# Kernel optimization log

Measured on AMD Instinct MI355X. Metric: run time of the kernel, lower is better.

## Reference

```python
import jax, jax.numpy as jnp
import numpy as np

GRID = 256
N_PTS = 500000

# 8 trilinear corner offsets
_OFFSETS = jnp.array([[0,0,0],[1,0,0],[0,1,0],[1,1,0],
                      [0,0,1],[1,0,1],[0,1,1],[1,1,1]], dtype=jnp.int32)


def setup_inputs() -> dict:
    key = jax.random.key(0)
    k1, k2 = jax.random.split(key)
    # match model init: means ~ N(0, 0.1), weights = |N(0,1)| (rand>=0 is equivalent post-relu)
    means = jax.random.normal(k1, (N_PTS, 3), dtype=jnp.float32) * 0.1
    weights = jax.random.uniform(k2, (N_PTS,), dtype=jnp.float32)
    sigma_param = jnp.ones((1,), dtype=jnp.float32)
    return {"means": means, "weights": weights, "sigma_param": sigma_param}


def _splat_trilinear(means, weights, grid_shape):
    factor = 0.5 * grid_shape
    grid_coords = means * factor + factor                      # [N,3]
    base = jax.lax.stop_gradient(jnp.floor(grid_coords).astype(jnp.int32))
    rem = grid_coords - base                                   # [N,3]
    # corner weights: prod over xyz of (rem if offset==1 else 1-rem) -> [N,8]
    terms = jnp.where(_OFFSETS[None, :, :] == 1, rem[:, None, :], 1.0 - rem[:, None, :])
    corner_w = jnp.prod(terms, axis=-1)                        # [N,8]
    vals = (corner_w * weights[:, None]).reshape(-1)           # [8N]
    idx = (base[:, None, :] + _OFFSETS[None, :, :]).reshape(-1, 3)  # [8N,3]
    grid = jnp.zeros((grid_shape, grid_shape, grid_shape), dtype=jnp.float32)
    # out-of-bounds indices are dropped by jax default scatter mode (same as original)
    return grid.at[idx[:, 0], idx[:, 1], idx[:, 2]].add(vals)


def _fft_blur(vol, sigma, grid_shape):
    d = h = w = grid_shape
    fz = jnp.fft.fftfreq(d)[:, None, None]
    fy = jnp.fft.fftfreq(h)[None, :, None]
    fx = jnp.fft.rfftfreq(w)[None, None, :]
    f_sq = (fz**2 + fy**2 + fx**2).astype(jnp.float32)         # [D,H,W//2+1]
    mask = jnp.exp(-2.0 * jnp.pi**2 * sigma**2 * f_sq)
    x = vol[None, ..., None]                                   # NDHWC
    spectrum = jnp.fft.rfftn(x, axes=(1, 2, 3))
    filtered = spectrum * mask[None, ..., None]
    out = jnp.fft.irfftn(filtered, s=(d, h, w), axes=(1, 2, 3))
    return out[0, ..., 0]


def reference(means, weights, sigma_param):
    w = jax.nn.relu(weights)
    sigma = jax.nn.relu(sigma_param)
    vol = _splat_trilinear(means, w, GRID)
    return _fft_blur(vol, sigma, GRID)
```

## Files before the change

kernel.cpp:

```cpp
#include <hip/hip_runtime.h>
#include <math.h>

#define GN 256
#define VOLN (GN * GN * GN)
#define VOLBYTES ((size_t)VOLN * sizeof(float))
#define RAD 16

#define CELLW 16
#define CPA   16
#define CELLS (CPA * CPA * CPA)
#define TILEW (CELLW + 1)
#define TILEN (TILEW * TILEW * TILEW)

#define HB  512
#define PPT 2
#define CHUNK 2048
#define MAXCHUNKS 4352

#define CCH 16

__device__ __forceinline__ int cell_of(float g0, float g1, float g2) {
    int b0 = (int)floorf(g0), b1 = (int)floorf(g1), b2 = (int)floorf(g2);
    b0 = min(max(b0, 0), 255); b1 = min(max(b1, 0), 255); b2 = min(max(b2, 0), 255);
    return ((b0 >> 4) << 8) | ((b1 >> 4) << 4) | (b2 >> 4);
}

__global__ __launch_bounds__(HB) void hist_kernel(const float* __restrict__ means,
                                                  unsigned* __restrict__ cellcnt, int n) {
    __shared__ unsigned lh[CELLS];
    int t = threadIdx.x;
    for (int i = t; i < CELLS; i += HB) lh[i] = 0u;
    __syncthreads();
    int base = blockIdx.x * (HB * PPT);
    for (int j = 0; j < PPT; ++j) {
        int p = base + j * HB + t;
        if (p < n) {
            float g0 = fmaf(means[3 * p + 0], 128.f, 128.f);
            float g1 = fmaf(means[3 * p + 1], 128.f, 128.f);
            float g2 = fmaf(means[3 * p + 2], 128.f, 128.f);
            atomicAdd(&lh[cell_of(g0, g1, g2)], 1u);
        }
    }
    __syncthreads();
    for (int i = t; i < CELLS; i += HB) {
        unsigned v = lh[i];
        if (v) atomicAdd(&cellcnt[i], v);
    }
}

__global__ __launch_bounds__(1024) void scan_kernel(const unsigned* __restrict__ cellcnt,
                                                    unsigned* __restrict__ cellstart,
                                                    unsigned* __restrict__ cursor,
                                                    uint4* __restrict__ desc) {
    __shared__ unsigned sums[1024];
    int t = threadIdx.x;
    unsigned c[4], loc[4], tot = 0u;
#pragma unroll
    for (int i = 0; i < 4; ++i) { c[i] = cellcnt[t * 4 + i]; loc[i] = tot; tot += c[i]; }
    sums[t] = tot;
    __syncthreads();
    for (int ofs = 1; ofs < 1024; ofs <<= 1) {
        unsigned v = (t >= ofs) ? sums[t - ofs] : 0u;
        __syncthreads();
        sums[t] += v;
        __syncthreads();
    }
    unsigned base = (t == 0) ? 0u : sums[t - 1];
    unsigned cs[4];
#pragma unroll
    for (int i = 0; i < 4; ++i) {
        cs[i] = base + loc[i];
        cellstart[t * 4 + i] = cs[i];
        cursor[t * 4 + i] = cs[i];
    }
    unsigned nch[4], lch[4], ctot = 0u;
#pragma unroll
    for (int i = 0; i < 4; ++i) { nch[i] = (c[i] + CHUNK - 1) / CHUNK; lch[i] = ctot; ctot += nch[i]; }
    __syncthreads();
    sums[t] = ctot;
    __syncthreads();
    for (int ofs = 1; ofs < 1024; ofs <<= 1) {
        unsigned v = (t >= ofs) ? sums[t - ofs] : 0u;
        __syncthreads();
        sums[t] += v;
        __syncthreads();
    }
    unsigned cbase = (t == 0) ? 0u : sums[t - 1];
#pragma unroll
    for (int i = 0; i < 4; ++i) {
        unsigned cb = cbase + lch[i];
        for (unsigned k = 0; k < nch[i]; ++k) {
            unsigned s0 = cs[i] + k * CHUNK;
            unsigned s1 = min(s0 + CHUNK, cs[i] + c[i]);
            desc[cb + k] = make_uint4((unsigned)(t * 4 + i), s0, s1, 0u);
        }
    }
    __syncthreads();
    unsigned total = sums[1023];
    for (unsigned i = total + t; i < MAXCHUNKS; i += 1024)
        desc[i] = make_uint4(0xFFFFFFFFu, 0u, 0u, 0u);
}

__global__ __launch_bounds__(HB) void scatter_kernel(const float* __restrict__ means,
                                                     const float* __restrict__ weights,
                                                     unsigned* __restrict__ cursor,
                                                     float4* __restrict__ sorted, int n) {
    __shared__ unsigned lh[CELLS];
    int t = threadIdx.x;
    for (int i = t; i < CELLS; i += HB) lh[i] = 0u;
    __syncthreads();
    int base = blockIdx.x * (HB * PPT);
    for (int j = 0; j < PPT; ++j) {
        int p = base + j * HB + t;
        if (p < n) {
            float g0 = fmaf(means[3 * p + 0], 128.f, 128.f);
            float g1 = fmaf(means[3 * p + 1], 128.f, 128.f);
            float g2 = fmaf(means[3 * p + 2], 128.f, 128.f);
            atomicAdd(&lh[cell_of(g0, g1, g2)], 1u);
        }
    }
    __syncthreads();
    for (int i = t; i < CELLS; i += HB) {
        unsigned v = lh[i];
        lh[i] = v ? atomicAdd(&cursor[i], v) : 0u;
    }
    __syncthreads();
    for (int j = 0; j < PPT; ++j) {
        int p = base + j * HB + t;
        if (p < n) {
            float g0 = fmaf(means[3 * p + 0], 128.f, 128.f);
            float g1 = fmaf(means[3 * p + 1], 128.f, 128.f);
            float g2 = fmaf(means[3 * p + 2], 128.f, 128.f);
            unsigned pos = atomicAdd(&lh[cell_of(g0, g1, g2)], 1u);
            sorted[pos] = make_float4(g0, g1, g2, fmaxf(weights[p], 0.f));
        }
    }
}

__global__ __launch_bounds__(256) void cellsplat_kernel(const float4* __restrict__ sorted,
                                                        const uint4* __restrict__ desc,
                                                        float* __restrict__ vol) {
    __shared__ float tile[TILEN];
    uint4 d = desc[blockIdx.x];
    if (d.x == 0xFFFFFFFFu) return;
    int c = (int)d.x;
    unsigned start = d.y, end = d.z;
    for (int i = threadIdx.x; i < TILEN; i += 256) tile[i] = 0.f;
    __syncthreads();
    int cb0 = (c >> 8) << 4, cb1 = ((c >> 4) & 15) << 4, cb2 = (c & 15) << 4;
    for (unsigned p0 = start; p0 < end; p0 += 256) {
        unsigned p = p0 + threadIdx.x;
        if (p < end) {
            float4 q = sorted[p];
            float f0 = floorf(q.x), f1 = floorf(q.y), f2 = floorf(q.z);
            int b0 = (int)f0, b1 = (int)f1, b2 = (int)f2;
            float r0 = q.x - f0, r1 = q.y - f1, r2 = q.z - f2;
            float c0v[2] = {1.f - r0, r0}, c1v[2] = {1.f - r1, r1}, c2v[2] = {1.f - r2, r2};
#pragma unroll
            for (int o0 = 0; o0 < 2; ++o0) {
                int v0 = b0 + o0, t0 = v0 - cb0;
                if ((unsigned)t0 > 16u || (unsigned)v0 > 255u) continue;
#pragma unroll
                for (int o1 = 0; o1 < 2; ++o1) {
                    int v1 = b1 + o1, t1 = v1 - cb1;
                    if ((unsigned)t1 > 16u || (unsigned)v1 > 255u) continue;
                    float w01 = c0v[o0] * c1v[o1] * q.w;
#pragma unroll
                    for (int o2 = 0; o2 < 2; ++o2) {
                        int v2 = b2 + o2, t2 = v2 - cb2;
                        if ((unsigned)t2 > 16u || (unsigned)v2 > 255u) continue;
                        atomicAdd(&tile[t0 * (TILEW * TILEW) + t1 * TILEW + t2], w01 * c2v[o2]);
                    }
                }
            }
        }
    }
    __syncthreads();
    for (int i = threadIdx.x; i < TILEN; i += 256) {
        float val = tile[i];
        if (val == 0.f) continue;
        int t0 = i / (TILEW * TILEW);
        int rem = i - t0 * (TILEW * TILEW);
        int t1 = rem / TILEW, t2 = rem - t1 * TILEW;
        int v0 = cb0 + t0, v1 = cb1 + t1, v2 = cb2 + t2;
        if (v0 < 256 && v1 < 256 && v2 < 256)
            atomicAdd(&vol[(v0 << 16) | (v1 << 8) | v2], val);
    }
}

__global__ __launch_bounds__(256) void taps_kernel(const float* __restrict__ sigma_param,
                                                   float* __restrict__ h) {
    __shared__ float red[4];
    int k = threadIdx.x;
    float s = fmaxf(sigma_param[0], 0.f);
    int kk = (k < 128) ? k : k - 256;
    float f = (float)kk / 256.f;
    float cc = 2.f * (float)(M_PI * M_PI) * s * s;
    float term = expf(-cc * f * f);
    int wid = k >> 6, lane = k & 63;
    for (int m = 0; m <= RAD; ++m) {
        int idx = (k * m) & 255;
        float v = term * cosf((float)idx * (2.f * (float)M_PI / 256.f));
#pragma unroll
        for (int o = 32; o > 0; o >>= 1) v += __shfl_down(v, o, 64);
        if (lane == 0) red[wid] = v;
        __syncthreads();
        if (k == 0) h[m] = (red[0] + red[1] + red[2] + red[3]) * (1.f / 256.f);
        __syncthreads();
    }
}

__global__ __launch_bounds__(256) void conv_d0_kernel(const float* __restrict__ in,
                                                      float* __restrict__ out,
                                                      const float* __restrict__ hh) {
    __shared__ float4 tile4[96][CCH];
    float shv[17];
#pragma unroll
    for (int j = 0; j < 17; ++j) shv[j] = hh[j];
    float taps[33];
#pragma unroll
    for (int m = 0; m < 33; ++m) taps[m] = shv[m < 16 ? 16 - m : m - 16];
    int i1 = blockIdx.x, t0 = blockIdx.y, ch = blockIdx.z;
    int colbase4 = ch * CCH;
    const float4* in4 = (const float4*)in;
#pragma unroll
    for (int it = 0; it < (96 * CCH) / 256; ++it) {
        int e = it * 256 + threadIdx.x;
        int r = e / CCH, cc = e % CCH;
        int i0 = ((t0 << 6) + r - 16) & 255;
        tile4[r][cc] = in4[(i0 << 14) | (i1 << 6) | (colbase4 + cc)];
    }
    __syncthreads();
    int cg = threadIdx.x & (CCH - 1);
    int r0 = threadIdx.x / CCH;
    for (int ro = 0; ro < 4; ++ro) {
        int rr = r0 + ro * 16;
        float4 acc = make_float4(0.f, 0.f, 0.f, 0.f);
#pragma unroll
        for (int m = 0; m < 33; ++m) {
            float4 v = tile4[rr + m][cg];
            acc.x = fmaf(taps[m], v.x, acc.x);
            acc.y = fmaf(taps[m], v.y, acc.y);
            acc.z = fmaf(taps[m], v.z, acc.z);
            acc.w = fmaf(taps[m], v.w, acc.w);
        }
        int o0 = (t0 << 6) + rr;
        ((float4*)out)[(o0 << 14) | (i1 << 6) | (colbase4 + cg)] = acc;
    }
}

__global__ __launch_bounds__(256) void conv_d1_kernel(const float* __restrict__ in,
                                                      float* __restrict__ out,
                                                      const float* __restrict__ hh) {
    __shared__ float4 tile4[96][CCH];
    float shv[17];
#pragma unroll
    for (int j = 0; j < 17; ++j) shv[j] = hh[j];
    float taps[33];
#pragma unroll
    for (int m = 0; m < 33; ++m) taps[m] = shv[m < 16 ? 16 - m : m - 16];
    int i0 = blockIdx.x, t1 = blockIdx.y, ch = blockIdx.z;
    int colbase4 = ch * CCH;
    const float4* in4 = (const float4*)in;
#pragma unroll
    for (int it = 0; it < (96 * CCH) / 256; ++it) {
        int e = it * 256 + threadIdx.x;
        int r = e / CCH, cc = e % CCH;
        int i1 = ((t1 << 6) + r - 16) & 255;
        tile4[r][cc] = in4[(i0 << 14) | (i1 << 6) | (colbase4 + cc)];
    }
    __syncthreads();
    int cg = threadIdx.x & (CCH - 1);
    int r0 = threadIdx.x / CCH;
    for (int ro = 0; ro < 4; ++ro) {
        int rr = r0 + ro * 16;
        float4 acc = make_float4(0.f, 0.f, 0.f, 0.f);
#pragma unroll
        for (int m = 0; m < 33; ++m) {
            float4 v = tile4[rr + m][cg];
            acc.x = fmaf(taps[m], v.x, acc.x);
            acc.y = fmaf(taps[m], v.y, acc.y);
            acc.z = fmaf(taps[m], v.z, acc.z);
            acc.w = fmaf(taps[m], v.w, acc.w);
        }
        int o1 = (t1 << 6) + rr;
        ((float4*)out)[(i0 << 14) | (o1 << 6) | (colbase4 + cg)] = acc;
    }
}

__global__ __launch_bounds__(256) void conv_d2_kernel(const float* __restrict__ in,
                                                      float* __restrict__ out,
                                                      const float* __restrict__ hh) {
    __shared__ float tile[4][256];
    float shv[17];
#pragma unroll
    for (int j = 0; j < 17; ++j) shv[j] = hh[j];
    int bx = blockIdx.x;
    size_t base = (size_t)bx * 1024;
#pragma unroll
    for (int it = 0; it < 4; ++it) {
        int e = it * 256 + threadIdx.x;
        ((float*)tile)[e] = in[base + e];
    }
    __syncthreads();
    int ri = threadIdx.x >> 6;
    int k = threadIdx.x & 63;
    const float4* row4 = (const float4*)tile[ri];
    float w[36];
#pragma unroll
    for (int j = 0; j < 9; ++j) {
        float4 q = row4[(k - 4 + j) & 63];
        w[4 * j + 0] = q.x; w[4 * j + 1] = q.y; w[4 * j + 2] = q.z; w[4 * j + 3] = q.w;
    }
    float acc[4] = {0.f, 0.f, 0.f, 0.f};
#pragma unroll
    for (int kk = 0; kk < 36; ++kk) {
#pragma unroll
        for (int i = 0; i < 4; ++i) {
            int d = kk - 16 - i;
            if (d >= -16 && d <= 16) acc[i] = fmaf(shv[d < 0 ? -d : d], w[kk], acc[i]);
        }
    }
    ((float4*)out)[(size_t)bx * 256 + ri * 64 + k] = make_float4(acc[0], acc[1], acc[2], acc[3]);
}

extern "C" void kernel_launch(void* const* d_in, const int* in_sizes, int n_in,
                              void* d_out, int out_size, void* d_ws, size_t ws_size,
                              hipStream_t stream) {
    const float* means   = (const float*)d_in[0];
    const float* weights = (const float*)d_in[1];
    const float* sigma   = (const float*)d_in[2];
    int n = in_sizes[1];

    float* vol = (float*)d_ws;
    float* h   = (float*)((char*)d_ws + VOLBYTES);
    float* out = (float*)d_out;

    char* ob = (char*)d_out;
    float4*   sorted    = (float4*)ob;
    unsigned* cellcnt   = (unsigned*)(ob + (8u << 20));
    unsigned* cellstart = (unsigned*)(ob + (8u << 20) + 65536);
    unsigned* cursor    = (unsigned*)(ob + (8u << 20) + 131072);
    uint4*    desc      = (uint4*)(ob + (9u << 20));

    hipMemsetAsync(vol, 0, VOLBYTES, stream);
    hipMemsetAsync(cellcnt, 0, CELLS * sizeof(unsigned), stream);
    taps_kernel<<<1, 256, 0, stream>>>(sigma, h);

    int nb = (n + HB * PPT - 1) / (HB * PPT);
    hist_kernel<<<nb, HB, 0, stream>>>(means, cellcnt, n);
    scan_kernel<<<1, 1024, 0, stream>>>(cellcnt, cellstart, cursor, desc);
    scatter_kernel<<<nb, HB, 0, stream>>>(means, weights, cursor, sorted, n);
    cellsplat_kernel<<<MAXCHUNKS, 256, 0, stream>>>(sorted, desc, vol);

    conv_d0_kernel<<<dim3(256, 4, 4), 256, 0, stream>>>(vol, out, h);
    conv_d1_kernel<<<dim3(256, 4, 4), 256, 0, stream>>>(out, vol, h);
    conv_d2_kernel<<<16384, 256, 0, stream>>>(vol, out, h);
}
```

Before: 244.9 us.

## Register-block depth convolutions over 8 outputs and widen cellsplat blocks

The d0/d1 convolution kernels now have each thread compute 8 consecutive outputs in registers, sliding over 40 shared-memory rows. This replaces 33 shared loads per output with 5 per output, which reduces LDS traffic. The tile is widened to 32 float4 columns and the grid z-dimension is halved to match. Cellsplat now launches 1024-thread blocks so each block processes more points at once. The cost is higher register pressure from 8 float4 accumulators plus 33 taps, and larger blocks in cellsplat may lower occupancy or increase contention on shared-memory atomics.

```diff
diff --git a/kernel.cpp b/kernel.cpp
--- a/kernel.cpp
+++ b/kernel.cpp
@@ -16,8 +16,9 @@
 #define PPT 2
 #define CHUNK 2048
 #define MAXCHUNKS 4352
-
-#define CCH 16
+#define SB  1024
+
+#define CCH 32
 
 __device__ __forceinline__ int cell_of(float g0, float g1, float g2) {
     int b0 = (int)floorf(g0), b1 = (int)floorf(g1), b2 = (int)floorf(g2);
@@ -137,18 +138,18 @@
     }
 }
 
-__global__ __launch_bounds__(256) void cellsplat_kernel(const float4* __restrict__ sorted,
-                                                        const uint4* __restrict__ desc,
-                                                        float* __restrict__ vol) {
+__global__ __launch_bounds__(SB) void cellsplat_kernel(const float4* __restrict__ sorted,
+                                                       const uint4* __restrict__ desc,
+                                                       float* __restrict__ vol) {
     __shared__ float tile[TILEN];
     uint4 d = desc[blockIdx.x];
     if (d.x == 0xFFFFFFFFu) return;
     int c = (int)d.x;
     unsigned start = d.y, end = d.z;
-    for (int i = threadIdx.x; i < TILEN; i += 256) tile[i] = 0.f;
+    for (int i = threadIdx.x; i < TILEN; i += SB) tile[i] = 0.f;
     __syncthreads();
     int cb0 = (c >> 8) << 4, cb1 = ((c >> 4) & 15) << 4, cb2 = (c & 15) << 4;
-    for (unsigned p0 = start; p0 < end; p0 += 256) {
+    for (unsigned p0 = start; p0 < end; p0 += SB) {
         unsigned p = p0 + threadIdx.x;
         if (p < end) {
             float4 q = sorted[p];
@@ -176,7 +177,7 @@
         }
     }
     __syncthreads();
-    for (int i = threadIdx.x; i < TILEN; i += 256) {
+    for (int i = threadIdx.x; i < TILEN; i += SB) {
         float val = tile[i];
         if (val == 0.f) continue;
         int t0 = i / (TILEW * TILEW);
@@ -226,26 +227,34 @@
 #pragma unroll
     for (int it = 0; it < (96 * CCH) / 256; ++it) {
         int e = it * 256 + threadIdx.x;
-        int r = e / CCH, cc = e % CCH;
+        int r = e >> 5, cc = e & 31;
         int i0 = ((t0 << 6) + r - 16) & 255;
         tile4[r][cc] = in4[(i0 << 14) | (i1 << 6) | (colbase4 + cc)];
     }
     __syncthreads();
-    int cg = threadIdx.x & (CCH - 1);
-    int r0 = threadIdx.x / CCH;
-    for (int ro = 0; ro < 4; ++ro) {
-        int rr = r0 + ro * 16;
-        float4 acc = make_float4(0.f, 0.f, 0.f, 0.f);
-#pragma unroll
-        for (int m = 0; m < 33; ++m) {
-            float4 v = tile4[rr + m][cg];
-            acc.x = fmaf(taps[m], v.x, acc.x);
-            acc.y = fmaf(taps[m], v.y, acc.y);
-            acc.z = fmaf(taps[m], v.z, acc.z);
-            acc.w = fmaf(taps[m], v.w, acc.w);
-        }
-        int o0 = (t0 << 6) + rr;
-        ((float4*)out)[(o0 << 14) | (i1 << 6) | (colbase4 + cg)] = acc;
+    int cg = threadIdx.x & 31;
+    int b = (threadIdx.x >> 5) << 3;
+    float4 acc[8];
+#pragma unroll
+    for (int j = 0; j < 8; ++j) acc[j] = make_float4(0.f, 0.f, 0.f, 0.f);
+#pragma unroll
+    for (int k = 0; k < 40; ++k) {
+        float4 v = tile4[b + k][cg];
+#pragma unroll
+        for (int j = 0; j < 8; ++j) {
+            if (k - j >= 0 && k - j <= 32) {
+                float tp = taps[k - j];
+                acc[j].x = fmaf(tp, v.x, acc[j].x);
+                acc[j].y = fmaf(tp, v.y, acc[j].y);
+                acc[j].z = fmaf(tp, v.z, acc[j].z);
+                acc[j].w = fmaf(tp, v.w, acc[j].w);
+            }
+        }
+    }
+#pragma unroll
+    for (int j = 0; j < 8; ++j) {
+        int o0 = (t0 << 6) + b + j;
+        ((float4*)out)[(o0 << 14) | (i1 << 6) | (colbase4 + cg)] = acc[j];
     }
 }
 
@@ -265,26 +274,34 @@
 #pragma unroll
     for (int it = 0; it < (96 * CCH) / 256; ++it) {
         int e = it * 256 + threadIdx.x;
-        int r = e / CCH, cc = e % CCH;
+        int r = e >> 5, cc = e & 31;
         int i1 = ((t1 << 6) + r - 16) & 255;
         tile4[r][cc] = in4[(i0 << 14) | (i1 << 6) | (colbase4 + cc)];
     }
     __syncthreads();
-    int cg = threadIdx.x & (CCH - 1);
-    int r0 = threadIdx.x / CCH;
-    for (int ro = 0; ro < 4; ++ro) {
-        int rr = r0 + ro * 16;
-        float4 acc = make_float4(0.f, 0.f, 0.f, 0.f);
-#pragma unroll
-        for (int m = 0; m < 33; ++m) {
-            float4 v = tile4[rr + m][cg];
-            acc.x = fmaf(taps[m], v.x, acc.x);
-            acc.y = fmaf(taps[m], v.y, acc.y);
-            acc.z = fmaf(taps[m], v.z, acc.z);
-            acc.w = fmaf(taps[m], v.w, acc.w);
-        }
-        int o1 = (t1 << 6) + rr;
-        ((float4*)out)[(i0 << 14) | (o1 << 6) | (colbase4 + cg)] = acc;
+    int cg = threadIdx.x & 31;
+    int b = (threadIdx.x >> 5) << 3;
+    float4 acc[8];
+#pragma unroll
+    for (int j = 0; j < 8; ++j) acc[j] = make_float4(0.f, 0.f, 0.f, 0.f);
+#pragma unroll
+    for (int k = 0; k < 40; ++k) {
+        float4 v = tile4[b + k][cg];
+#pragma unroll
+        for (int j = 0; j < 8; ++j) {
+            if (k - j >= 0 && k - j <= 32) {
+                float tp = taps[k - j];
+                acc[j].x = fmaf(tp, v.x, acc[j].x);
+                acc[j].y = fmaf(tp, v.y, acc[j].y);
+                acc[j].z = fmaf(tp, v.z, acc[j].z);
+                acc[j].w = fmaf(tp, v.w, acc[j].w);
+            }
+        }
+    }
+#pragma unroll
+    for (int j = 0; j < 8; ++j) {
+        int o1 = (t1 << 6) + b + j;
+        ((float4*)out)[(i0 << 14) | (o1 << 6) | (colbase4 + cg)] = acc[j];
     }
 }
 
@@ -351,9 +368,9 @@
     hist_kernel<<<nb, HB, 0, stream>>>(means, cellcnt, n);
     scan_kernel<<<1, 1024, 0, stream>>>(cellcnt, cellstart, cursor, desc);
     scatter_kernel<<<nb, HB, 0, stream>>>(means, weights, cursor, sorted, n);
-    cellsplat_kernel<<<MAXCHUNKS, 256, 0, stream>>>(sorted, desc, vol);
-
-    conv_d0_kernel<<<dim3(256, 4, 4), 256, 0, stream>>>(vol, out, h);
-    conv_d1_kernel<<<dim3(256, 4, 4), 256, 0, stream>>>(out, vol, h);
+    cellsplat_kernel<<<MAXCHUNKS, SB, 0, stream>>>(sorted, desc, vol);
+
+    conv_d0_kernel<<<dim3(256, 4, 2), 256, 0, stream>>>(vol, out, h);
+    conv_d1_kernel<<<dim3(256, 4, 2), 256, 0, stream>>>(out, vol, h);
     conv_d2_kernel<<<16384, 256, 0, stream>>>(vol, out, h);
 }
```

Result: faster. 239.7 us (-2.1%).
